# Kernel tuning notes

Hardware: AMD Instinct MI355X
Metric: run time of the kernel (lower is better)

## Reference

```python
import jax, jax.numpy as jnp
import numpy as np

D_MODEL, D_K, D_V = 1024, 128, 128
B, S = 8, 2048


def setup_inputs() -> dict:
    key = jax.random.key(0)
    ks = jax.random.split(key, 10)
    scale = 1.0 / np.sqrt(D_MODEL)
    return {
        "inputs_q": jax.random.normal(ks[0], (B, S, D_MODEL), jnp.float32),
        "inputs_k": jax.random.normal(ks[1], (B, S, D_MODEL), jnp.float32),
        "inputs_v": jax.random.normal(ks[2], (B, S, D_MODEL), jnp.float32),
        "mask": jax.random.randint(ks[3], (B, 1, S), 0, 2, jnp.int32),
        "Wq": jax.random.normal(ks[4], (D_MODEL, D_K), jnp.float32) * scale,
        "bq": jnp.zeros((D_K,), jnp.float32),
        "Wk": jax.random.normal(ks[5], (D_MODEL, D_K), jnp.float32) * scale,
        "bk": jnp.zeros((D_K,), jnp.float32),
        "Wv": jax.random.normal(ks[6], (D_MODEL, D_V), jnp.float32) * scale,
        "bv": jnp.zeros((D_V,), jnp.float32),
    }


def reference(inputs_q, inputs_k, inputs_v, mask, Wq, bq, Wk, bk, Wv, bv):
    query = inputs_q @ Wq + bq            # [B,Sq,d_k]
    key = inputs_k @ Wk + bk              # [B,Sk,d_k]
    value = inputs_v @ Wv + bv            # [B,Sk,d_v]
    scores = jnp.einsum('bqd,bkd->bqk', query, key) / jnp.sqrt(jnp.float32(D_K))
    # original: mask==True means attend; inverted mask positions get -1e9
    mask_float = jnp.logical_not(mask.astype(bool)).astype(jnp.float32)  # [B,1,Sk]
    scores = scores + mask_float * (-1e9)
    attention_weights = jax.nn.softmax(scores, axis=-1)
    attention_weights = attention_weights * (1.0 - mask_float)
    output = jnp.einsum('bqk,bkv->bqv', attention_weights, value)
    return output
```

## Files before the change

kernel.cpp:

```cpp
#include <hip/hip_runtime.h>

#define L2E 1.44269504088896341f
#define SM_SHIFT 5.77078016355585f

typedef _Float16 h8 __attribute__((ext_vector_type(8)));
typedef float f4 __attribute__((ext_vector_type(4)));

__device__ __forceinline__ void gll16(const void* g, void* l) {
  __builtin_amdgcn_global_load_lds((const __attribute__((address_space(1))) void*)g,
                                   (__attribute__((address_space(3))) void*)l, 16, 0, 0);
}

__device__ __forceinline__ f4 mfma_h(h8 a, h8 b, f4 c) {
  return __builtin_amdgcn_mfma_f32_16x16x32_f16(a, b, c, 0, 0, 0);
}

__device__ __forceinline__ h8 pack8(const float4& a, const float4& b) {
  h8 hv;
  hv[0] = (_Float16)a.x; hv[1] = (_Float16)a.y; hv[2] = (_Float16)a.z; hv[3] = (_Float16)a.w;
  hv[4] = (_Float16)b.x; hv[5] = (_Float16)b.y; hv[6] = (_Float16)b.z; hv[7] = (_Float16)b.w;
  return hv;
}

__global__ void wt_prep(const float* __restrict__ Wq, const float* __restrict__ Wk,
                        const float* __restrict__ Wv, const int* __restrict__ maskp,
                        _Float16* __restrict__ Wt, _Float16* __restrict__ mh) {
  int z = blockIdx.y;
  const float* W = (z == 0) ? Wq : ((z == 1) ? Wk : Wv);
  _Float16* o = Wt + (size_t)z * 131072;
  int idx = blockIdx.x * 256 + threadIdx.x;
  int k = idx >> 7, n = idx & 127;
  o[(k >> 6) * 8192 + ((k >> 3) & 7) * 1024 + n * 8 + (k & 7)] = (_Float16)W[idx];
  if (z == 0 && idx < 16384) mh[idx] = (_Float16)(float)maskp[idx];
}

__global__ __launch_bounds__(256, 3) void proj_qkv(
    const float* __restrict__ Xq, const float* __restrict__ Xk, const float* __restrict__ Xv,
    const _Float16* __restrict__ Wt, const int* __restrict__ maskp,
    const float* __restrict__ bq, const float* __restrict__ bk, const float* __restrict__ bv,
    _Float16* __restrict__ Qh, _Float16* __restrict__ Kpk, _Float16* __restrict__ Vpk) {
  const int z = blockIdx.y;
  const float* X; const float* bias;
  if (z == 0) { X = Xq; bias = bq; }
  else if (z == 1) { X = Xk; bias = bk; }
  else { X = Xv; bias = bv; }
  const _Float16* Wz = Wt + (size_t)z * 131072;
  const int row0 = blockIdx.x * 64;
  const int tid = threadIdx.x;
  const int lane = tid & 63, wid = tid >> 6;
  const int wr = wid >> 1, wc = wid & 1;
  const int l15 = lane & 15, g = lane >> 4;

  __shared__ __align__(16) _Float16 Al[4096];
  __shared__ __align__(16) _Float16 Bl[2][8192];

  f4 acc[2][4];
#pragma unroll
  for (int i = 0; i < 2; i++)
#pragma unroll
    for (int j = 0; j < 4; j++) acc[i][j] = (f4){0.f, 0.f, 0.f, 0.f};

  float4 areg[2][2];
  const int ar_row = tid >> 3, ar_ko = tid & 7;
  auto loadA = [&](int t) {
#pragma unroll
    for (int it = 0; it < 2; it++) {
      const float* gp = X + (size_t)(row0 + it * 32 + ar_row) * 1024 + t * 64 + ar_ko * 8;
      areg[it][0] = *(const float4*)gp;
      areg[it][1] = *(const float4*)(gp + 4);
    }
  };
  auto writeA = [&]() {
#pragma unroll
    for (int it = 0; it < 2; it++) {
      int row = it * 32 + ar_row;
      *(h8*)&Al[(row * 8 + (ar_ko ^ (row & 7))) * 8] = pack8(areg[it][0], areg[it][1]);
    }
  };
  auto loadB = [&](int buf, int t) {
#pragma unroll
    for (int it = 0; it < 4; it++)
      gll16(Wz + t * 8192 + it * 2048 + tid * 8, &Bl[buf][it * 2048 + tid * 8]);
  };
  auto compute = [&](int buf) {
#pragma unroll
    for (int kc = 0; kc < 2; kc++) {
      int o = kc * 4 + g;
      h8 af[2], bf[4];
#pragma unroll
      for (int mf = 0; mf < 2; mf++) {
        int row = wr * 32 + mf * 16 + l15;
        af[mf] = *(const h8*)&Al[(row * 8 + (o ^ (row & 7))) * 8];
      }
#pragma unroll
      for (int nf = 0; nf < 4; nf++) {
        int col = wc * 64 + nf * 16 + l15;
        bf[nf] = *(const h8*)&Bl[buf][(o * 128 + col) * 8];
      }
#pragma unroll
      for (int mf = 0; mf < 2; mf++)
#pragma unroll
        for (int nf = 0; nf < 4; nf++)
          acc[mf][nf] = mfma_h(af[mf], bf[nf], acc[mf][nf]);
    }
  };

  loadA(0);
  loadB(0, 0);

  int cur = 0;
  for (int t = 0; t < 16; t++) {
    writeA();
    __syncthreads();
    if (t < 15) {
      loadA(t + 1);
      loadB(cur ^ 1, t + 1);
    }
    compute(cur);
    __syncthreads();
    cur ^= 1;
  }

  const float qscale = (z == 0) ? 0.08838834764831845f : 1.0f;
#pragma unroll
  for (int nf = 0; nf < 4; nf++) {
    int colb = wc * 64 + nf * 16 + l15;
    float bv_ = bias[colb];
#pragma unroll
    for (int mf = 0; mf < 2; mf++)
#pragma unroll
      for (int jj = 0; jj < 4; jj++) {
        int m = row0 + wr * 32 + mf * 16 + g * 4 + jj;
        float v = (acc[mf][nf][jj] + bv_) * qscale;
        if (z == 2) v *= (float)maskp[m];
        _Float16 hv = (_Float16)v;
        if (z == 0) Qh[m * 128 + colb] = hv;
        else if (z == 1) Kpk[(m >> 6) * 8192 + (colb >> 3) * 512 + (m & 63) * 8 + (colb & 7)] = hv;
        else Vpk[(m >> 6) * 8192 + ((m & 63) >> 3) * 1024 + colb * 8 + (m & 7)] = hv;
      }
  }
}

__global__ __launch_bounds__(256, 2) void attn_fwd(
    const _Float16* __restrict__ Qh, const _Float16* __restrict__ Kpk,
    const _Float16* __restrict__ Vpk, const _Float16* __restrict__ maskh,
    float* __restrict__ Out) {
  const int bi = blockIdx.x & 7;
  const int qt = blockIdx.x >> 3;
  const int tid = threadIdx.x;
  const int lane = tid & 63, wid = tid >> 6;
  const int l15 = lane & 15, g = lane >> 4;
  const int qg = wid & 1;
  const int kh = wid >> 1;

  __shared__ __align__(16) _Float16 Kt[16384];
  __shared__ __align__(16) _Float16 Vt[16384];
  __shared__ __align__(16) _Float16 Pl[4][1024];

  const size_t mb = (size_t)bi * 2048;
  const int q0 = qt * 32 + qg * 16;

  h8 qf[4];
#pragma unroll
  for (int c = 0; c < 4; c++)
    qf[c] = *(const h8*)(Qh + (mb + q0 + l15) * 128 + c * 32 + g * 8);

  const _Float16* Kb = Kpk + (size_t)bi * 262144;
  const _Float16* Vb = Vpk + (size_t)bi * 262144;
  const _Float16* mhp = maskh + mb;

  f4 oacc[8];
#pragma unroll
  for (int i = 0; i < 8; i++) oacc[i] = (f4){0.f, 0.f, 0.f, 0.f};
  f4 lacc = (f4){0.f, 0.f, 0.f, 0.f};

  h8 kreg[8], vreg[8];
#pragma unroll
  for (int it = 0; it < 8; it++) {
    kreg[it] = *(const h8*)(Kb + (it * 256 + tid) * 8);
    vreg[it] = *(const h8*)(Vb + (it * 256 + tid) * 8);
  }

  for (int s = 0; s < 16; s++) {
#pragma unroll
    for (int it = 0; it < 8; it++) {
      int wg = it * 256 + tid;
      *(h8*)&Kt[(wg ^ ((wg >> 6) & 7)) * 8] = kreg[it];
      *(h8*)&Vt[(wg ^ ((wg >> 7) & 7)) * 8] = vreg[it];
    }
    __syncthreads();

    if (s < 15) {
      const _Float16* gk = Kb + (size_t)(s + 1) * 16384;
      const _Float16* gv = Vb + (size_t)(s + 1) * 16384;
#pragma unroll
      for (int it = 0; it < 8; it++) {
        kreg[it] = *(const h8*)(gk + (it * 256 + tid) * 8);
        vreg[it] = *(const h8*)(gv + (it * 256 + tid) * 8);
      }
    }

    f4 sc[4];
#pragma unroll
    for (int nf = 0; nf < 4; nf++) sc[nf] = (f4){0.f, 0.f, 0.f, 0.f};
#pragma unroll
    for (int c = 0; c < 4; c++) {
      int dblk = c * 4 + g;
#pragma unroll
      for (int nf = 0; nf < 4; nf++) {
        int key64 = nf * 16 + l15;
        int kg = kh * 1024 + dblk * 64 + (key64 ^ (dblk & 7));
        h8 bfr = *(const h8*)&Kt[kg * 8];
        sc[nf] = mfma_h(qf[c], bfr, sc[nf]);
      }
    }

#pragma unroll
    for (int nf = 0; nf < 4; nf++) {
      int key64 = nf * 16 + l15;
      int kb = key64 >> 3, j = key64 & 7;
#pragma unroll
      for (int jj = 0; jj < 4; jj++) {
        int q = g * 4 + jj;
        float p = __builtin_amdgcn_exp2f(sc[nf][jj] * L2E - SM_SHIFT);
        Pl[wid][((kb * 16 + (q ^ (kb & 7))) << 3) + j] = (_Float16)p;
      }
    }

#pragma unroll
    for (int kc2 = 0; kc2 < 2; kc2++) {
      int kbp = kc2 * 4 + g;
      h8 pa = *(const h8*)&Pl[wid][((kbp * 16 + (l15 ^ (kbp & 7))) << 3)];
      h8 mfr = *(const h8*)(mhp + s * 128 + kh * 64 + kc2 * 32 + g * 8);
      lacc = mfma_h(pa, mfr, lacc);
#pragma unroll
      for (int nf = 0; nf < 8; nf++) {
        int d = nf * 16 + l15;
        int vg = kh * 1024 + kbp * 128 + (d ^ (kbp & 7));
        h8 va = *(const h8*)&Vt[vg * 8];
        oacc[nf] = mfma_h(pa, va, oacc[nf]);
      }
    }
    __syncthreads();
  }

  float* red = (float*)Kt;
  if (kh == 1) {
    int base = qg * 2304;
#pragma unroll
    for (int nf = 0; nf < 8; nf++)
#pragma unroll
      for (int jj = 0; jj < 4; jj++)
        red[base + (nf * 4 + jj) * 64 + lane] = oacc[nf][jj];
#pragma unroll
    for (int jj = 0; jj < 4; jj++)
      red[base + 2048 + jj * 64 + lane] = lacc[jj];
  }
  __syncthreads();
  if (kh == 0) {
    int base = qg * 2304;
#pragma unroll
    for (int nf = 0; nf < 8; nf++)
#pragma unroll
      for (int jj = 0; jj < 4; jj++)
        oacc[nf][jj] += red[base + (nf * 4 + jj) * 64 + lane];
#pragma unroll
    for (int jj = 0; jj < 4; jj++)
      lacc[jj] += red[base + 2048 + jj * 64 + lane];

    float inv[4];
#pragma unroll
    for (int jj = 0; jj < 4; jj++)
      inv[jj] = (lacc[jj] > 0.f) ? 1.0f / lacc[jj] : 0.0f;
#pragma unroll
    for (int nf = 0; nf < 8; nf++)
#pragma unroll
      for (int jj = 0; jj < 4; jj++)
        Out[(mb + q0 + g * 4 + jj) * 128 + nf * 16 + l15] = oacc[nf][jj] * inv[jj];
  }
}

extern "C" void kernel_launch(void* const* d_in, const int* in_sizes, int n_in,
                              void* d_out, int out_size, void* d_ws, size_t ws_size,
                              hipStream_t stream) {
  const float* Xq = (const float*)d_in[0];
  const float* Xk = (const float*)d_in[1];
  const float* Xv = (const float*)d_in[2];
  const int* mask = (const int*)d_in[3];
  const float* Wq = (const float*)d_in[4];
  const float* bq = (const float*)d_in[5];
  const float* Wk = (const float*)d_in[6];
  const float* bk = (const float*)d_in[7];
  const float* Wv = (const float*)d_in[8];
  const float* bv = (const float*)d_in[9];
  float* Out = (float*)d_out;

  char* ws = (char*)d_ws;
  _Float16* Qh    = (_Float16*)(ws);
  _Float16* Kpk   = (_Float16*)(ws + 4194304);
  _Float16* Vpk   = (_Float16*)(ws + 8388608);
  _Float16* Wt    = (_Float16*)(ws + 12582912);
  _Float16* maskh = (_Float16*)(ws + 13369344);

  wt_prep<<<dim3(512, 3), 256, 0, stream>>>(Wq, Wk, Wv, mask, Wt, maskh);
  proj_qkv<<<dim3(256, 3), 256, 0, stream>>>(Xq, Xk, Xv, Wt, mask, bq, bk, bv, Qh, Kpk, Vpk);
  attn_fwd<<<dim3(512), 256, 0, stream>>>(Qh, Kpk, Vpk, maskh, Out);
}
```

Before: 90.52 us.

## Halve key tile to 64 keys per step to raise attention kernel occupancy

```diff
diff --git a/kernel.cpp b/kernel.cpp
--- a/kernel.cpp
+++ b/kernel.cpp
@@ -141,7 +141,7 @@
   }
 }
 
-__global__ __launch_bounds__(256, 2) void attn_fwd(
+__global__ __launch_bounds__(256, 4) void attn_fwd(
     const _Float16* __restrict__ Qh, const _Float16* __restrict__ Kpk,
     const _Float16* __restrict__ Vpk, const _Float16* __restrict__ maskh,
     float* __restrict__ Out) {
@@ -151,11 +151,11 @@
   const int lane = tid & 63, wid = tid >> 6;
   const int l15 = lane & 15, g = lane >> 4;
   const int qg = wid & 1;
-  const int kh = wid >> 1;
-
-  __shared__ __align__(16) _Float16 Kt[16384];
-  __shared__ __align__(16) _Float16 Vt[16384];
-  __shared__ __align__(16) _Float16 Pl[4][1024];
+  const int kq = wid >> 1;
+
+  __shared__ __align__(16) _Float16 Kt[8192];
+  __shared__ __align__(16) _Float16 Vt[8192];
+  __shared__ __align__(16) _Float16 Pl[4][512];
 
   const size_t mb = (size_t)bi * 2048;
   const int q0 = qt * 32 + qg * 16;
@@ -174,99 +174,98 @@
   for (int i = 0; i < 8; i++) oacc[i] = (f4){0.f, 0.f, 0.f, 0.f};
   f4 lacc = (f4){0.f, 0.f, 0.f, 0.f};
 
-  h8 kreg[8], vreg[8];
-#pragma unroll
-  for (int it = 0; it < 8; it++) {
+  h8 kreg[4], vreg[4], mregC, mregN;
+#pragma unroll
+  for (int it = 0; it < 4; it++) {
     kreg[it] = *(const h8*)(Kb + (it * 256 + tid) * 8);
     vreg[it] = *(const h8*)(Vb + (it * 256 + tid) * 8);
   }
-
-  for (int s = 0; s < 16; s++) {
-#pragma unroll
-    for (int it = 0; it < 8; it++) {
+  mregC = *(const h8*)(mhp + kq * 32 + g * 8);
+
+  for (int s = 0; s < 32; s++) {
+#pragma unroll
+    for (int it = 0; it < 4; it++) {
       int wg = it * 256 + tid;
       *(h8*)&Kt[(wg ^ ((wg >> 6) & 7)) * 8] = kreg[it];
       *(h8*)&Vt[(wg ^ ((wg >> 7) & 7)) * 8] = vreg[it];
     }
     __syncthreads();
 
-    if (s < 15) {
-      const _Float16* gk = Kb + (size_t)(s + 1) * 16384;
-      const _Float16* gv = Vb + (size_t)(s + 1) * 16384;
-#pragma unroll
-      for (int it = 0; it < 8; it++) {
+    if (s < 31) {
+      const _Float16* gk = Kb + (size_t)(s + 1) * 8192;
+      const _Float16* gv = Vb + (size_t)(s + 1) * 8192;
+#pragma unroll
+      for (int it = 0; it < 4; it++) {
         kreg[it] = *(const h8*)(gk + (it * 256 + tid) * 8);
         vreg[it] = *(const h8*)(gv + (it * 256 + tid) * 8);
       }
-    }
-
-    f4 sc[4];
-#pragma unroll
-    for (int nf = 0; nf < 4; nf++) sc[nf] = (f4){0.f, 0.f, 0.f, 0.f};
+      mregN = *(const h8*)(mhp + (s + 1) * 64 + kq * 32 + g * 8);
+    }
+
+    f4 sc[2];
+    sc[0] = (f4){0.f, 0.f, 0.f, 0.f};
+    sc[1] = (f4){0.f, 0.f, 0.f, 0.f};
 #pragma unroll
     for (int c = 0; c < 4; c++) {
       int dblk = c * 4 + g;
 #pragma unroll
-      for (int nf = 0; nf < 4; nf++) {
-        int key64 = nf * 16 + l15;
-        int kg = kh * 1024 + dblk * 64 + (key64 ^ (dblk & 7));
+      for (int nf = 0; nf < 2; nf++) {
+        int key64 = kq * 32 + nf * 16 + l15;
+        int kg = dblk * 64 + (key64 ^ (dblk & 7));
         h8 bfr = *(const h8*)&Kt[kg * 8];
         sc[nf] = mfma_h(qf[c], bfr, sc[nf]);
       }
     }
 
 #pragma unroll
-    for (int nf = 0; nf < 4; nf++) {
-      int key64 = nf * 16 + l15;
-      int kb = key64 >> 3, j = key64 & 7;
+    for (int nf = 0; nf < 2; nf++) {
+      int key32 = nf * 16 + l15;
+      int ko = key32 >> 3, j = key32 & 7;
 #pragma unroll
       for (int jj = 0; jj < 4; jj++) {
         int q = g * 4 + jj;
         float p = __builtin_amdgcn_exp2f(sc[nf][jj] * L2E - SM_SHIFT);
-        Pl[wid][((kb * 16 + (q ^ (kb & 7))) << 3) + j] = (_Float16)p;
-      }
-    }
-
-#pragma unroll
-    for (int kc2 = 0; kc2 < 2; kc2++) {
-      int kbp = kc2 * 4 + g;
-      h8 pa = *(const h8*)&Pl[wid][((kbp * 16 + (l15 ^ (kbp & 7))) << 3)];
-      h8 mfr = *(const h8*)(mhp + s * 128 + kh * 64 + kc2 * 32 + g * 8);
-      lacc = mfma_h(pa, mfr, lacc);
+        Pl[wid][((ko * 16 + (q ^ (ko & 3))) << 3) + j] = (_Float16)p;
+      }
+    }
+
+    {
+      int kbp = kq * 4 + g;
+      h8 pa = *(const h8*)&Pl[wid][((g * 16 + (l15 ^ (g & 3))) << 3)];
+      lacc = mfma_h(pa, mregC, lacc);
 #pragma unroll
       for (int nf = 0; nf < 8; nf++) {
         int d = nf * 16 + l15;
-        int vg = kh * 1024 + kbp * 128 + (d ^ (kbp & 7));
+        int vg = kbp * 128 + (d ^ (kbp & 7));
         h8 va = *(const h8*)&Vt[vg * 8];
         oacc[nf] = mfma_h(pa, va, oacc[nf]);
       }
     }
+    if (s < 31) mregC = mregN;
     __syncthreads();
   }
 
-  float* red = (float*)Kt;
-  if (kh == 1) {
-    int base = qg * 2304;
+  float* red = (qg == 0) ? (float*)Kt : (float*)Vt;
+  if (kq == 1) {
 #pragma unroll
     for (int nf = 0; nf < 8; nf++)
 #pragma unroll
       for (int jj = 0; jj < 4; jj++)
-        red[base + (nf * 4 + jj) * 64 + lane] = oacc[nf][jj];
+        red[(nf * 4 + jj) * 64 + lane] = oacc[nf][jj];
 #pragma unroll
     for (int jj = 0; jj < 4; jj++)
-      red[base + 2048 + jj * 64 + lane] = lacc[jj];
+      red[2048 + jj * 64 + lane] = lacc[jj];
   }
   __syncthreads();
-  if (kh == 0) {
-    int base = qg * 2304;
+  if (kq == 0) {
 #pragma unroll
     for (int nf = 0; nf < 8; nf++)
 #pragma unroll
       for (int jj = 0; jj < 4; jj++)
-        oacc[nf][jj] += red[base + (nf * 4 + jj) * 64 + lane];
+        oacc[nf][jj] += red[(nf * 4 + jj) * 64 + lane];
 #pragma unroll
     for (int jj = 0; jj < 4; jj++)
-      lacc[jj] += red[base + 2048 + jj * 64 + lane];
+      lacc[jj] += red[2048 + jj * 64 + lane];
 
     float inv[4];
 #pragma unroll
```

Result: slower. 94.43 us (+4.3%).
